# Performance work log

Hardware: AMD Instinct MI355X
Metric: run time of the kernel (lower is better)

Reference implementation:

```python
import jax, jax.numpy as jnp
import numpy as np
import math

NH = 16  # n_head
HS = 64  # head_size = n_embd // n_head


def setup_inputs() -> dict:
    key = jax.random.key(0)
    ks = jax.random.split(key, 7)
    B, T, C, QL, KVL = 2, 2048, 1024, 128, 128
    s = lambda k, shape, fan_in: jax.random.normal(k, shape, jnp.float32) / np.sqrt(fan_in)
    return {
        "x": jax.random.normal(ks[0], (B, T, C), jnp.float32),
        "W_dq": s(ks[1], (QL, C), C),
        "W_uq": s(ks[2], (C, QL), QL),
        "W_dkv": s(ks[3], (KVL, C), C),
        "W_uk": s(ks[4], (C, KVL), KVL),
        "W_uv": s(ks[5], (C, KVL), KVL),
        "W_o": s(ks[6], (C, C), C),
    }


def reference(x, W_dq, W_uq, W_dkv, W_uk, W_uv, W_o):
    B, T, C = x.shape
    kvl = W_dkv.shape[0]
    # absorbed matrices (training branch)
    k_eff = (W_dq.T @ W_uq.T @ W_uk).reshape(NH, HS, kvl)            # (nh, hs, kvl)
    v_eff = (W_uv.T @ W_o.T).reshape(kvl, NH, HS).transpose(1, 0, 2)  # (nh, kvl, hs)
    # latent kv cache
    c_kv = x @ W_dkv.T                                                # (B, T, kvl)
    # query path
    q = (x @ W_dq.T @ W_uq.T).reshape(B, T, NH, HS).transpose(0, 2, 1, 3)  # (B, nh, T, hs)
    # scores: q @ k_eff @ c_kv^T
    ql = jnp.einsum('bhtd,hdl->bhtl', q, k_eff)                       # (B, nh, T, kvl)
    scores = jnp.einsum('bhtl,bsl->bhts', ql, c_kv) / math.sqrt(HS)   # (B, nh, T, T)
    # causal mask
    mask = jnp.tril(jnp.ones((T, T), dtype=bool))
    scores = jnp.where(mask[None, None], scores, -jnp.inf)
    attn = jax.nn.softmax(scores, axis=-1)
    # output: attn @ c_kv @ v_eff
    ctx = jnp.einsum('bhts,bsl->bhtl', attn, c_kv)                    # (B, nh, T, kvl)
    y = jnp.einsum('bhtl,hld->bhtd', ctx, v_eff)                      # (B, nh, T, hs)
    y = y.transpose(0, 2, 1, 3).reshape(B, T, C)
    return y, c_kv
```

## Files before the change

### kernel.cpp

```cpp
#include <hip/hip_runtime.h>
#include <hip/hip_bf16.h>

typedef __hip_bfloat16 bf16;
typedef __attribute__((ext_vector_type(8))) short short8;
typedef __attribute__((ext_vector_type(4))) float f32x4;

#define NHD 16
#define HSD 64
#define KVLD 128
#define QLD 128
#define CD 1024
#define BD 2
#define TD 2048

__device__ __forceinline__ short8 ld8(const bf16* p) { return *(const short8*)p; }
__device__ __forceinline__ void st8(bf16* p, short8 v) { *(short8*)p = v; }

__device__ __forceinline__ short8 cvt8(float4 a, float4 b) {
    union { short8 s; bf16 h[8]; } u;
    u.h[0] = __float2bfloat16(a.x); u.h[1] = __float2bfloat16(a.y);
    u.h[2] = __float2bfloat16(a.z); u.h[3] = __float2bfloat16(a.w);
    u.h[4] = __float2bfloat16(b.x); u.h[5] = __float2bfloat16(b.y);
    u.h[6] = __float2bfloat16(b.z); u.h[7] = __float2bfloat16(b.w);
    return u.s;
}
__device__ __forceinline__ void st4(bf16* p, float4 a) {
    union { short4 s; bf16 h[4]; } u;
    u.h[0] = __float2bfloat16(a.x); u.h[1] = __float2bfloat16(a.y);
    u.h[2] = __float2bfloat16(a.z); u.h[3] = __float2bfloat16(a.w);
    *(short4*)p = u.s;
}
__device__ __forceinline__ void st4f(bf16* p, f32x4 a) {
    union { short4 s; bf16 h[4]; } u;
    u.h[0] = __float2bfloat16(a[0]); u.h[1] = __float2bfloat16(a[1]);
    u.h[2] = __float2bfloat16(a[2]); u.h[3] = __float2bfloat16(a[3]);
    *(short4*)p = u.s;
}


__global__ __launch_bounds__(256) void k_m1p(const float* __restrict__ wuq,
                                             const float* __restrict__ wuk,
                                             float* __restrict__ m1p) {
    int idx = blockIdx.x * 256 + threadIdx.x;
    int i = idx >> 7, j = idx & 127;
    int c0 = blockIdx.y * 128;
    float acc = 0.f;
    for (int c = c0; c < c0 + 128; ++c)
        acc += wuq[c * QLD + i] * wuk[c * KVLD + j];
    m1p[blockIdx.y * 16384 + idx] = acc;
}

__global__ __launch_bounds__(256) void k_m1r(const float* __restrict__ m1p,
                                             float* __restrict__ m1) {
    int idx = blockIdx.x * 256 + threadIdx.x;
    float acc = 0.f;
#pragma unroll
    for (int p = 0; p < 8; ++p) acc += m1p[p * 16384 + idx];
    m1[idx] = acc;
}

__global__ __launch_bounds__(256) void k_keff(const float* __restrict__ wdq,
                                              const float* __restrict__ m1,
                                              float* __restrict__ keff) {
    int idx = blockIdx.x * 256 + threadIdx.x;
    int c = idx >> 7, j = idx & 127;
    float acc = 0.f;
    for (int i = 0; i < QLD; ++i)
        acc += wdq[i * CD + c] * m1[i * KVLD + j];
    keff[idx] = acc;
}

__global__ __launch_bounds__(256) void k_veff(const float* __restrict__ wuv,
                                              const float* __restrict__ wo,
                                              bf16* __restrict__ veffT_bf) {
    int idx = blockIdx.x * 256 + threadIdx.x;
    int l = idx & 127;
    int cc = idx >> 7;
    float acc = 0.f;
    for (int c0 = 0; c0 < CD; ++c0)
        acc += wuv[c0 * KVLD + l] * wo[(size_t)cc * CD + c0];
    veffT_bf[idx] = __float2bfloat16(acc);
}

__global__ __launch_bounds__(256) void k_E(const float* __restrict__ wuq,
                                           const float* __restrict__ keff,
                                           bf16* __restrict__ Et_bf) {
    int idx = blockIdx.x * 256 + threadIdx.x;
    int i = idx & 127;
    int l = (idx >> 7) & 127;
    int h = idx >> 14;
    float acc = 0.f;
    for (int d = 0; d < HSD; ++d)
        acc += wuq[(h * HSD + d) * QLD + i] * keff[(h * HSD + d) * KVLD + l];
    Et_bf[idx] = __float2bfloat16(0.1803368801f * acc);
}

__global__ __launch_bounds__(256) void k_proj(const float* __restrict__ x,
                                              const float* __restrict__ wdq,
                                              const float* __restrict__ wdkv,
                                              bf16* __restrict__ q1_bf,
                                              float* __restrict__ ckv_out,
                                              bf16* __restrict__ ckv_bf,
                                              bf16* __restrict__ ckvT_bf) {
    const int m0 = blockIdx.x * 16;
    const int tid = threadIdx.x;
    const int w = tid >> 6, lane = tid & 63, m16 = lane & 15, g = lane >> 4;

    __shared__ __align__(16) short As_raw[16 * 72];
    __shared__ __align__(16) short Bs_raw[256 * 72];
    bf16* As = (bf16*)As_raw;
    bf16* Bs = (bf16*)Bs_raw;

    f32x4 acc[4];
#pragma unroll
    for (int nb = 0; nb < 4; ++nb) acc[nb] = (f32x4){0.f, 0.f, 0.f, 0.f};

    for (int k0 = 0; k0 < CD; k0 += 64) {
        __syncthreads();
        {
            int row = tid >> 4, kc = (tid & 15) << 2;
            float4 f = *(const float4*)(x + (size_t)(m0 + row) * CD + k0 + kc);
            st4(As + row * 72 + kc, f);
        }
#pragma unroll
        for (int kk = 0; kk < 8; ++kk) {
            int v = tid + kk * 256;
            int row = v >> 3, kc = (v & 7) << 3;
            const float* wr = (row < 128) ? (wdq + (size_t)row * CD)
                                          : (wdkv + (size_t)(row - 128) * CD);
            const float* src = wr + k0 + kc;
            float4 f0 = *(const float4*)(src);
            float4 f1 = *(const float4*)(src + 4);
            st8(Bs + row * 72 + kc, cvt8(f0, f1));
        }
        __syncthreads();
        short8 aF[2];
#pragma unroll
        for (int kf = 0; kf < 2; ++kf)
            aF[kf] = ld8(As + m16 * 72 + kf * 32 + g * 8);
#pragma unroll
        for (int nb = 0; nb < 4; ++nb)
#pragma unroll
            for (int kf = 0; kf < 2; ++kf) {
                short8 bF = ld8(Bs + (w * 64 + nb * 16 + m16) * 72 + kf * 32 + g * 8);
                acc[nb] = __builtin_amdgcn_mfma_f32_16x16x32_bf16(aF[kf], bF, acc[nb], 0, 0, 0);
            }
    }

#pragma unroll
    for (int nb = 0; nb < 4; ++nb)
#pragma unroll
        for (int r = 0; r < 4; ++r) {
            int t = m0 + g * 4 + r;
            int col = w * 64 + nb * 16 + m16;
            float v = acc[nb][r];
            if (col < 128) {
                q1_bf[(size_t)t * QLD + col] = __float2bfloat16(v);
            } else {
                int l = col - 128;
                ckv_out[(size_t)t * KVLD + l] = v;
                bf16 hv = __float2bfloat16(v);
                ckv_bf[(size_t)t * KVLD + l] = hv;
                int b = t >> 11, tl = t & 2047;
                ckvT_bf[((size_t)b * KVLD + l) * TD + tl] = hv;
            }
        }
}

__global__ __launch_bounds__(512, 4) void k_flash(const bf16* __restrict__ Q1_bf,
                                                  const bf16* __restrict__ Et_bf,
                                                  const bf16* __restrict__ ckv_bf,
                                                  const bf16* __restrict__ ckvT_bf,
                                                  const bf16* __restrict__ veffT_bf,
                                                  float* __restrict__ yout) {
    const int h = blockIdx.x & 15;
    const int b = blockIdx.x >> 4;
    const int qlo = blockIdx.y;
    const int qhi = 31 - qlo;
    const int tid = threadIdx.x;
    const int w = tid >> 6;
    const int ws = w >> 2;
    const int wq = w & 3;
    const int lane = tid & 63;
    const int m16 = lane & 15;
    const int g = lane >> 4;
    const int myqt = ws ? qlo : qhi;
    const int row0 = myqt * 64;

    __shared__ __align__(16) short smem_raw[28288];
    bf16* smem = (bf16*)smem_raw;
    bf16* kvN = smem;
    bf16* kvT = smem + 8704;
    bf16* pS  = smem + 19072 + w * 1152;
    bf16* bufLo = kvT;
    bf16* vT = smem + 19072;

    {
        const bf16 one = __float2bfloat16(1.0f);
        for (int idx = tid; idx < 16 * 72; idx += 512)
            kvT[9216 + idx] = one;
    }

    {
        const bf16* q1hi = Q1_bf + ((size_t)(b * TD + qhi * 64)) * QLD;
        const bf16* q1lo = Q1_bf + ((size_t)(b * TD + qlo * 64)) * QLD;
#pragma unroll
        for (int k = 0; k < 2; ++k) {
            int v = tid + k * 512;
            int row = v >> 4, cv = (v & 15) << 3;
            st8(kvN + row * 136 + cv, ld8(q1hi + row * QLD + cv));
            st8(bufLo + row * 136 + cv, ld8(q1lo + row * QLD + cv));
        }
    }
    __syncthreads();
    bf16* myQ1 = ws ? bufLo : kvN;
    {
        short8 aq[4];
#pragma unroll
        for (int kf = 0; kf < 4; ++kf)
            aq[kf] = ld8(myQ1 + (wq * 16 + m16) * 136 + kf * 32 + g * 8);
        const bf16* Eh = Et_bf + (size_t)h * QLD * KVLD;
        f32x4 qc[8];
#pragma unroll
        for (int nb = 0; nb < 8; ++nb) qc[nb] = (f32x4){0.f, 0.f, 0.f, 0.f};
#pragma unroll
        for (int nb = 0; nb < 8; ++nb)
#pragma unroll
            for (int kf = 0; kf < 4; ++kf) {
                short8 bq = ld8(Eh + (nb * 16 + m16) * QLD + kf * 32 + g * 8);
                qc[nb] = __builtin_amdgcn_mfma_f32_16x16x32_bf16(aq[kf], bq, qc[nb], 0, 0, 0);
            }
        __syncthreads();
#pragma unroll
        for (int nb = 0; nb < 8; ++nb)
#pragma unroll
            for (int r = 0; r < 4; ++r)
                myQ1[(wq * 16 + g * 4 + r) * 136 + nb * 16 + m16] = __float2bfloat16(qc[nb][r]);
    }
    __syncthreads();
    short8 qlA[4];
#pragma unroll
    for (int kf = 0; kf < 4; ++kf)
        qlA[kf] = ld8(myQ1 + (wq * 16 + m16) * 136 + kf * 32 + g * 8);

    f32x4 cx[9];
#pragma unroll
    for (int nb = 0; nb < 9; ++nb) cx[nb] = (f32x4){0.f, 0.f, 0.f, 0.f};
    float mrow = -INFINITY;
    const int rg = row0 + wq * 16 + m16;

    const bf16* ckb = ckv_bf + (size_t)b * TD * KVLD;
    const bf16* ckTb = ckvT_bf + (size_t)b * KVLD * TD;

    int nrow[2], ncol[2], trow[2], tcol[2];
#pragma unroll
    for (int k = 0; k < 2; ++k) {
        int v = tid + k * 512;
        nrow[k] = v >> 4; ncol[k] = (v & 15) << 3;
        trow[k] = v >> 3; tcol[k] = (v & 7) << 3;
    }
    short8 pfN[2], pfT[2];
#pragma unroll
    for (int k = 0; k < 2; ++k) {
        pfN[k] = ld8(ckb + (size_t)nrow[k] * KVLD + ncol[k]);
        pfT[k] = ld8(ckTb + (size_t)trow[k] * TD + tcol[k]);
    }

    for (int tile = 0; tile <= qhi; ++tile) {
        const int s0 = tile * 64;
        __syncthreads();
#pragma unroll
        for (int k = 0; k < 2; ++k) {
            st8(kvN + nrow[k] * 136 + ncol[k], pfN[k]);
            st8(kvT + trow[k] * 72 + tcol[k], pfT[k]);
        }
        __syncthreads();
        if (tile < qhi) {
            const int s1 = s0 + 64;
#pragma unroll
            for (int k = 0; k < 2; ++k) {
                pfN[k] = ld8(ckb + (size_t)(s1 + nrow[k]) * KVLD + ncol[k]);
                pfT[k] = ld8(ckTb + (size_t)trow[k] * TD + s1 + tcol[k]);
            }
        }

        if (ws == 0 || tile <= qlo) {
            f32x4 sa[4];
#pragma unroll
            for (int nb = 0; nb < 4; ++nb) sa[nb] = (f32x4){0.f, 0.f, 0.f, 0.f};
#pragma unroll
            for (int nb = 0; nb < 4; ++nb)
#pragma unroll
                for (int kf = 0; kf < 4; ++kf) {
                    short8 ak = ld8(kvN + (nb * 16 + m16) * 136 + kf * 32 + g * 8);
                    sa[nb] = __builtin_amdgcn_mfma_f32_16x16x32_bf16(ak, qlA[kf], sa[nb], 0, 0, 0);
                }

            if (tile == myqt) {
#pragma unroll
                for (int nb = 0; nb < 4; ++nb)
#pragma unroll
                    for (int r = 0; r < 4; ++r) {
                        int sg = s0 + nb * 16 + g * 4 + r;
                        if (sg > rg) sa[nb][r] = -INFINITY;
                    }
            }

            float mloc = sa[0][0];
#pragma unroll
            for (int nb = 0; nb < 4; ++nb)
#pragma unroll
                for (int r = 0; r < 4; ++r) mloc = fmaxf(mloc, sa[nb][r]);
            mloc = fmaxf(mloc, __shfl_xor(mloc, 16));
            mloc = fmaxf(mloc, __shfl_xor(mloc, 32));
            if (__any(mloc > mrow)) {
                float mt = fmaxf(mrow, mloc);
                float al = exp2f(mrow - mt);
                mrow = mt;
#pragma unroll
                for (int nb = 0; nb < 9; ++nb)
#pragma unroll
                    for (int r = 0; r < 4; ++r) cx[nb][r] *= al;
            }

#pragma unroll
            for (int nb = 0; nb < 4; ++nb) {
                float4 p4;
                p4.x = exp2f(sa[nb][0] - mrow);
                p4.y = exp2f(sa[nb][1] - mrow);
                p4.z = exp2f(sa[nb][2] - mrow);
                p4.w = exp2f(sa[nb][3] - mrow);
                st4(pS + m16 * 72 + nb * 16 + g * 4, p4);
            }
            __builtin_amdgcn_wave_barrier();

            short8 pA[2];
#pragma unroll
            for (int kf = 0; kf < 2; ++kf)
                pA[kf] = ld8(pS + m16 * 72 + kf * 32 + g * 8);
#pragma unroll
            for (int nb = 0; nb < 9; ++nb)
#pragma unroll
                for (int kf = 0; kf < 2; ++kf) {
                    short8 av = ld8(kvT + (nb * 16 + m16) * 72 + kf * 32 + g * 8);
                    cx[nb] = __builtin_amdgcn_mfma_f32_16x16x32_bf16(av, pA[kf], cx[nb], 0, 0, 0);
                }
        }
    }

    float invl = 1.f / cx[8][0];
#pragma unroll
    for (int nb = 0; nb < 8; ++nb)
#pragma unroll
        for (int r = 0; r < 4; ++r) cx[nb][r] *= invl;
    __syncthreads();
    bf16* ctxS = ws ? bufLo : kvN;
#pragma unroll
    for (int nb = 0; nb < 8; ++nb)
        st4f(ctxS + (wq * 16 + m16) * 136 + nb * 16 + g * 4, cx[nb]);
    {
        const bf16* vsrc = veffT_bf + (size_t)h * HSD * KVLD;
#pragma unroll
        for (int k = 0; k < 2; ++k) {
            int v = tid + k * 512;
            int row = v >> 4, cv = (v & 15) << 3;
            st8(vT + row * 136 + cv, ld8(vsrc + row * KVLD + cv));
        }
    }
    __syncthreads();

    short8 cB[4];
#pragma unroll
    for (int kf = 0; kf < 4; ++kf)
        cB[kf] = ld8(ctxS + (wq * 16 + m16) * 136 + kf * 32 + g * 8);
    f32x4 ya[4];
#pragma unroll
    for (int nb = 0; nb < 4; ++nb) ya[nb] = (f32x4){0.f, 0.f, 0.f, 0.f};
#pragma unroll
    for (int nb = 0; nb < 4; ++nb)
#pragma unroll
        for (int kf = 0; kf < 4; ++kf) {
            short8 av = ld8(vT + (nb * 16 + m16) * 136 + kf * 32 + g * 8);
            ya[nb] = __builtin_amdgcn_mfma_f32_16x16x32_bf16(av, cB[kf], ya[nb], 0, 0, 0);
        }
    float* yo = yout + ((size_t)b * TD + rg) * CD + h * HSD;
#pragma unroll
    for (int nb = 0; nb < 4; ++nb)
        *(float4*)(yo + nb * 16 + g * 4) = *(float4*)&ya[nb];
}

extern "C" void kernel_launch(void* const* d_in, const int* in_sizes, int n_in,
                              void* d_out, int out_size, void* d_ws, size_t ws_size,
                              hipStream_t stream) {
    const float* x    = (const float*)d_in[0];
    const float* wdq  = (const float*)d_in[1];
    const float* wuq  = (const float*)d_in[2];
    const float* wdkv = (const float*)d_in[3];
    const float* wuk  = (const float*)d_in[4];
    const float* wuv  = (const float*)d_in[5];
    const float* wo   = (const float*)d_in[6];
    float* yout = (float*)d_out;
    float* ckv_out = yout + (size_t)BD * TD * CD;

    float* ws = (float*)d_ws;
    float* M1   = ws;
    float* M1P  = M1 + 16384;
    float* keff = M1P + 131072;
    bf16* Et_bf    = (bf16*)(keff + 131072);
    bf16* veffT_bf = Et_bf + 262144;
    bf16* ckv_bf   = veffT_bf + 131072;
    bf16* ckvT_bf  = ckv_bf + 524288;
    bf16* Q1_bf    = ckvT_bf + 524288;

    dim3 m1grid(64, 8);
    k_m1p <<<m1grid, 256, 0, stream>>>(wuq, wuk, M1P);
    k_m1r <<<64,   256, 0, stream>>>(M1P, M1);
    k_keff<<<512,  256, 0, stream>>>(wdq, M1, keff);
    k_veff<<<512,  256, 0, stream>>>(wuv, wo, veffT_bf);
    k_E   <<<1024, 256, 0, stream>>>(wuq, keff, Et_bf);

    k_proj<<<TD * BD / 16, 256, 0, stream>>>(x, wdq, wdkv, Q1_bf, ckv_out, ckv_bf, ckvT_bf);

    dim3 grid(32, 16);
    k_flash<<<grid, 512, 0, stream>>>(Q1_bf, Et_bf, ckv_bf, ckvT_bf, veffT_bf, yout);
}
```

Before: 263.7 us.

## Fuse weight-absorption prologue kernels into two launches and reassociate E computation

Replaces the six prologue kernels (M1 partials, reduction, k_eff, v_eff, E, projection) with two launches. One kernel computes M1 partials, a per-head G = W_dq-slice·W_uq product, and a bf16 copy of W_dq/W_dkv. The second kernel runs the projection, the E matrix and v_eff concurrently as different block ranges. E is reassociated so the full k_eff is never formed, and the projection now reads weights that were converted to bf16 beforehand. This cuts launch count and serial dependencies and uses register-blocked vector loads. The cost is block-role branching and a different floating-point summation order.

```diff
diff --git a/kernel.cpp b/kernel.cpp
--- a/kernel.cpp
+++ b/kernel.cpp
@@ -16,14 +16,6 @@
 __device__ __forceinline__ short8 ld8(const bf16* p) { return *(const short8*)p; }
 __device__ __forceinline__ void st8(bf16* p, short8 v) { *(short8*)p = v; }
 
-__device__ __forceinline__ short8 cvt8(float4 a, float4 b) {
-    union { short8 s; bf16 h[8]; } u;
-    u.h[0] = __float2bfloat16(a.x); u.h[1] = __float2bfloat16(a.y);
-    u.h[2] = __float2bfloat16(a.z); u.h[3] = __float2bfloat16(a.w);
-    u.h[4] = __float2bfloat16(b.x); u.h[5] = __float2bfloat16(b.y);
-    u.h[6] = __float2bfloat16(b.z); u.h[7] = __float2bfloat16(b.w);
-    return u.s;
-}
 __device__ __forceinline__ void st4(bf16* p, float4 a) {
     union { short4 s; bf16 h[4]; } u;
     u.h[0] = __float2bfloat16(a.x); u.h[1] = __float2bfloat16(a.y);
@@ -37,134 +29,190 @@
     *(short4*)p = u.s;
 }
 
-
-__global__ __launch_bounds__(256) void k_m1p(const float* __restrict__ wuq,
+__global__ __launch_bounds__(256) void k_pre(const float* __restrict__ wuq,
                                              const float* __restrict__ wuk,
-                                             float* __restrict__ m1p) {
-    int idx = blockIdx.x * 256 + threadIdx.x;
-    int i = idx >> 7, j = idx & 127;
-    int c0 = blockIdx.y * 128;
-    float acc = 0.f;
-    for (int c = c0; c < c0 + 128; ++c)
-        acc += wuq[c * QLD + i] * wuk[c * KVLD + j];
-    m1p[blockIdx.y * 16384 + idx] = acc;
-}
-
-__global__ __launch_bounds__(256) void k_m1r(const float* __restrict__ m1p,
-                                             float* __restrict__ m1) {
-    int idx = blockIdx.x * 256 + threadIdx.x;
-    float acc = 0.f;
-#pragma unroll
-    for (int p = 0; p < 8; ++p) acc += m1p[p * 16384 + idx];
-    m1[idx] = acc;
-}
-
-__global__ __launch_bounds__(256) void k_keff(const float* __restrict__ wdq,
-                                              const float* __restrict__ m1,
-                                              float* __restrict__ keff) {
-    int idx = blockIdx.x * 256 + threadIdx.x;
-    int c = idx >> 7, j = idx & 127;
-    float acc = 0.f;
-    for (int i = 0; i < QLD; ++i)
-        acc += wdq[i * CD + c] * m1[i * KVLD + j];
-    keff[idx] = acc;
-}
-
-__global__ __launch_bounds__(256) void k_veff(const float* __restrict__ wuv,
+                                             const float* __restrict__ wdq,
+                                             const float* __restrict__ wdkv,
+                                             float* __restrict__ m1p,
+                                             float* __restrict__ G,
+                                             bf16* __restrict__ wqkv_bf) {
+    const int b = blockIdx.x;
+    const int tid = threadIdx.x;
+    if (b < 32) {
+        const int part = b >> 2, iq = b & 3;
+        const int i = iq * 32 + (tid >> 3);
+        const int j16 = (tid & 7) << 4;
+        float acc[16];
+#pragma unroll
+        for (int t = 0; t < 16; ++t) acc[t] = 0.f;
+        const float* wq = wuq + (size_t)part * 128 * QLD;
+        const float* wk = wuk + (size_t)part * 128 * KVLD;
+#pragma unroll 2
+        for (int c = 0; c < 128; ++c) {
+            float a = wq[c * QLD + i];
+            const float4* wr = (const float4*)(wk + c * KVLD + j16);
+            float4 b0 = wr[0], b1 = wr[1], b2 = wr[2], b3 = wr[3];
+            acc[0] += a * b0.x;  acc[1] += a * b0.y;  acc[2] += a * b0.z;  acc[3] += a * b0.w;
+            acc[4] += a * b1.x;  acc[5] += a * b1.y;  acc[6] += a * b1.z;  acc[7] += a * b1.w;
+            acc[8] += a * b2.x;  acc[9] += a * b2.y;  acc[10] += a * b2.z; acc[11] += a * b2.w;
+            acc[12] += a * b3.x; acc[13] += a * b3.y; acc[14] += a * b3.z; acc[15] += a * b3.w;
+        }
+        float* dst = m1p + (size_t)part * 16384 + (size_t)i * 128 + j16;
+#pragma unroll
+        for (int q = 0; q < 4; ++q)
+            ((float4*)dst)[q] = make_float4(acc[4 * q], acc[4 * q + 1], acc[4 * q + 2], acc[4 * q + 3]);
+    } else if (b < 96) {
+        const int b1 = b - 32;
+        const int h = b1 >> 2, pq = b1 & 3;
+        const int p = pq * 32 + (tid >> 3);
+        const int i16 = (tid & 7) << 4;
+        float acc[16];
+#pragma unroll
+        for (int t = 0; t < 16; ++t) acc[t] = 0.f;
+        const float* wdqp = wdq + (size_t)p * CD + h * 64;
+        const float* wuqh = wuq + (size_t)(h * 64) * QLD + i16;
+#pragma unroll 2
+        for (int d = 0; d < 64; ++d) {
+            float a = wdqp[d];
+            const float4* wr = (const float4*)(wuqh + d * QLD);
+            float4 b0 = wr[0], b1v = wr[1], b2 = wr[2], b3 = wr[3];
+            acc[0] += a * b0.x;  acc[1] += a * b0.y;  acc[2] += a * b0.z;  acc[3] += a * b0.w;
+            acc[4] += a * b1v.x; acc[5] += a * b1v.y; acc[6] += a * b1v.z; acc[7] += a * b1v.w;
+            acc[8] += a * b2.x;  acc[9] += a * b2.y;  acc[10] += a * b2.z; acc[11] += a * b2.w;
+            acc[12] += a * b3.x; acc[13] += a * b3.y; acc[14] += a * b3.z; acc[15] += a * b3.w;
+        }
+        float* dst = G + (size_t)h * 16384 + (size_t)p * 128 + i16;
+#pragma unroll
+        for (int q = 0; q < 4; ++q)
+            ((float4*)dst)[q] = make_float4(acc[4 * q], acc[4 * q + 1], acc[4 * q + 2], acc[4 * q + 3]);
+    } else {
+        const int r = (b - 96) * 16 + (tid >> 4);
+        const int c0 = (tid & 15) << 6;
+        const float* src = (r < 128) ? (wdq + (size_t)r * CD) : (wdkv + (size_t)(r - 128) * CD);
+#pragma unroll
+        for (int t = 0; t < 16; ++t) {
+            float4 f = *(const float4*)(src + c0 + t * 4);
+            st4(wqkv_bf + (size_t)r * CD + c0 + t * 4, f);
+        }
+    }
+}
+
+__global__ __launch_bounds__(256) void k_main(const float* __restrict__ x,
+                                              const bf16* __restrict__ wqkv_bf,
+                                              const float* __restrict__ m1p,
+                                              const float* __restrict__ G,
+                                              const float* __restrict__ wuv,
                                               const float* __restrict__ wo,
-                                              bf16* __restrict__ veffT_bf) {
-    int idx = blockIdx.x * 256 + threadIdx.x;
-    int l = idx & 127;
-    int cc = idx >> 7;
-    float acc = 0.f;
-    for (int c0 = 0; c0 < CD; ++c0)
-        acc += wuv[c0 * KVLD + l] * wo[(size_t)cc * CD + c0];
-    veffT_bf[idx] = __float2bfloat16(acc);
-}
-
-__global__ __launch_bounds__(256) void k_E(const float* __restrict__ wuq,
-                                           const float* __restrict__ keff,
-                                           bf16* __restrict__ Et_bf) {
-    int idx = blockIdx.x * 256 + threadIdx.x;
-    int i = idx & 127;
-    int l = (idx >> 7) & 127;
-    int h = idx >> 14;
-    float acc = 0.f;
-    for (int d = 0; d < HSD; ++d)
-        acc += wuq[(h * HSD + d) * QLD + i] * keff[(h * HSD + d) * KVLD + l];
-    Et_bf[idx] = __float2bfloat16(0.1803368801f * acc);
-}
-
-__global__ __launch_bounds__(256) void k_proj(const float* __restrict__ x,
-                                              const float* __restrict__ wdq,
-                                              const float* __restrict__ wdkv,
                                               bf16* __restrict__ q1_bf,
                                               float* __restrict__ ckv_out,
                                               bf16* __restrict__ ckv_bf,
-                                              bf16* __restrict__ ckvT_bf) {
-    const int m0 = blockIdx.x * 16;
-    const int tid = threadIdx.x;
-    const int w = tid >> 6, lane = tid & 63, m16 = lane & 15, g = lane >> 4;
-
+                                              bf16* __restrict__ ckvT_bf,
+                                              bf16* __restrict__ Et_bf,
+                                              bf16* __restrict__ veffT_bf) {
     __shared__ __align__(16) short As_raw[16 * 72];
     __shared__ __align__(16) short Bs_raw[256 * 72];
-    bf16* As = (bf16*)As_raw;
-    bf16* Bs = (bf16*)Bs_raw;
-
-    f32x4 acc[4];
-#pragma unroll
-    for (int nb = 0; nb < 4; ++nb) acc[nb] = (f32x4){0.f, 0.f, 0.f, 0.f};
-
-    for (int k0 = 0; k0 < CD; k0 += 64) {
+    __shared__ float m1s[1024];
+    const int blk = blockIdx.x;
+    const int tid = threadIdx.x;
+
+    if (blk < 256) {
+        const int m0 = blk * 16;
+        const int w = tid >> 6, lane = tid & 63, m16 = lane & 15, g = lane >> 4;
+        bf16* As = (bf16*)As_raw;
+        bf16* Bs = (bf16*)Bs_raw;
+
+        f32x4 acc[4];
+#pragma unroll
+        for (int nb = 0; nb < 4; ++nb) acc[nb] = (f32x4){0.f, 0.f, 0.f, 0.f};
+
+        for (int k0 = 0; k0 < CD; k0 += 64) {
+            __syncthreads();
+            {
+                int row = tid >> 4, kc = (tid & 15) << 2;
+                float4 f = *(const float4*)(x + (size_t)(m0 + row) * CD + k0 + kc);
+                st4(As + row * 72 + kc, f);
+            }
+#pragma unroll
+            for (int kk = 0; kk < 8; ++kk) {
+                int v = tid + kk * 256;
+                int row = v >> 3, kc = (v & 7) << 3;
+                st8(Bs + row * 72 + kc, ld8(wqkv_bf + (size_t)row * CD + k0 + kc));
+            }
+            __syncthreads();
+            short8 aF[2];
+#pragma unroll
+            for (int kf = 0; kf < 2; ++kf)
+                aF[kf] = ld8(As + m16 * 72 + kf * 32 + g * 8);
+#pragma unroll
+            for (int nb = 0; nb < 4; ++nb)
+#pragma unroll
+                for (int kf = 0; kf < 2; ++kf) {
+                    short8 bF = ld8(Bs + (w * 64 + nb * 16 + m16) * 72 + kf * 32 + g * 8);
+                    acc[nb] = __builtin_amdgcn_mfma_f32_16x16x32_bf16(aF[kf], bF, acc[nb], 0, 0, 0);
+                }
+        }
+
+#pragma unroll
+        for (int nb = 0; nb < 4; ++nb)
+#pragma unroll
+            for (int r = 0; r < 4; ++r) {
+                int t = m0 + g * 4 + r;
+                int col = w * 64 + nb * 16 + m16;
+                float v = acc[nb][r];
+                if (col < 128) {
+                    q1_bf[(size_t)t * QLD + col] = __float2bfloat16(v);
+                } else {
+                    int l = col - 128;
+                    ckv_out[(size_t)t * KVLD + l] = v;
+                    bf16 hv = __float2bfloat16(v);
+                    ckv_bf[(size_t)t * KVLD + l] = hv;
+                    int b = t >> 11, tl = t & 2047;
+                    ckvT_bf[((size_t)b * KVLD + l) * TD + tl] = hv;
+                }
+            }
+    } else if (blk < 512) {
+        const int b2 = blk - 256;
+        const int h = b2 >> 4, lb = b2 & 15;
+        for (int v = tid; v < 1024; v += 256) {
+            int p = v >> 3, lq = v & 7;
+            float s = 0.f;
+#pragma unroll
+            for (int part = 0; part < 8; ++part)
+                s += m1p[(size_t)part * 16384 + (size_t)p * 128 + lb * 8 + lq];
+            m1s[v] = s;
+        }
         __syncthreads();
-        {
-            int row = tid >> 4, kc = (tid & 15) << 2;
-            float4 f = *(const float4*)(x + (size_t)(m0 + row) * CD + k0 + kc);
-            st4(As + row * 72 + kc, f);
-        }
-#pragma unroll
-        for (int kk = 0; kk < 8; ++kk) {
-            int v = tid + kk * 256;
-            int row = v >> 3, kc = (v & 7) << 3;
-            const float* wr = (row < 128) ? (wdq + (size_t)row * CD)
-                                          : (wdkv + (size_t)(row - 128) * CD);
-            const float* src = wr + k0 + kc;
-            float4 f0 = *(const float4*)(src);
-            float4 f1 = *(const float4*)(src + 4);
-            st8(Bs + row * 72 + kc, cvt8(f0, f1));
-        }
-        __syncthreads();
-        short8 aF[2];
-#pragma unroll
-        for (int kf = 0; kf < 2; ++kf)
-            aF[kf] = ld8(As + m16 * 72 + kf * 32 + g * 8);
-#pragma unroll
-        for (int nb = 0; nb < 4; ++nb)
-#pragma unroll
-            for (int kf = 0; kf < 2; ++kf) {
-                short8 bF = ld8(Bs + (w * 64 + nb * 16 + m16) * 72 + kf * 32 + g * 8);
-                acc[nb] = __builtin_amdgcn_mfma_f32_16x16x32_bf16(aF[kf], bF, acc[nb], 0, 0, 0);
-            }
-    }
-
-#pragma unroll
-    for (int nb = 0; nb < 4; ++nb)
-#pragma unroll
-        for (int r = 0; r < 4; ++r) {
-            int t = m0 + g * 4 + r;
-            int col = w * 64 + nb * 16 + m16;
-            float v = acc[nb][r];
-            if (col < 128) {
-                q1_bf[(size_t)t * QLD + col] = __float2bfloat16(v);
-            } else {
-                int l = col - 128;
-                ckv_out[(size_t)t * KVLD + l] = v;
-                bf16 hv = __float2bfloat16(v);
-                ckv_bf[(size_t)t * KVLD + l] = hv;
-                int b = t >> 11, tl = t & 2047;
-                ckvT_bf[((size_t)b * KVLD + l) * TD + tl] = hv;
-            }
-        }
+        const int lq = tid >> 5, i4 = (tid & 31) << 2;
+        const float* Gh = G + (size_t)h * 16384;
+        float4 acc = make_float4(0.f, 0.f, 0.f, 0.f);
+#pragma unroll 4
+        for (int p = 0; p < 128; ++p) {
+            float a = m1s[p * 8 + lq];
+            float4 g4 = *(const float4*)(Gh + p * 128 + i4);
+            acc.x += a * g4.x; acc.y += a * g4.y;
+            acc.z += a * g4.z; acc.w += a * g4.w;
+        }
+        const float sc = 0.1803368801f;
+        const int l = lb * 8 + lq;
+        st4(Et_bf + ((size_t)h * 128 + l) * 128 + i4,
+            make_float4(sc * acc.x, sc * acc.y, sc * acc.z, sc * acc.w));
+    } else {
+        const int b3 = blk - 512;
+        const int cc = b3 * 4 + (tid >> 6);
+        const int l2 = (tid & 63) << 1;
+        const float* wor = wo + (size_t)cc * CD;
+        float ax = 0.f, ay = 0.f;
+#pragma unroll 4
+        for (int c0 = 0; c0 < CD; ++c0) {
+            float a = wor[c0];
+            float2 wv = *(const float2*)(wuv + (size_t)c0 * KVLD + l2);
+            ax += a * wv.x; ay += a * wv.y;
+        }
+        union { short2 s; bf16 h2[2]; } u;
+        u.h2[0] = __float2bfloat16(ax);
+        u.h2[1] = __float2bfloat16(ay);
+        *(short2*)(veffT_bf + (size_t)cc * KVLD + l2) = u.s;
+    }
 }
 
 __global__ __launch_bounds__(512, 4) void k_flash(const bf16* __restrict__ Q1_bf,
@@ -403,23 +451,18 @@
     float* ckv_out = yout + (size_t)BD * TD * CD;
 
     float* ws = (float*)d_ws;
-    float* M1   = ws;
-    float* M1P  = M1 + 16384;
-    float* keff = M1P + 131072;
-    bf16* Et_bf    = (bf16*)(keff + 131072);
+    float* M1P = ws;
+    float* G   = M1P + 131072;
+    bf16* wqkv_bf  = (bf16*)(G + 262144);
+    bf16* Et_bf    = wqkv_bf + 262144;
     bf16* veffT_bf = Et_bf + 262144;
     bf16* ckv_bf   = veffT_bf + 131072;
     bf16* ckvT_bf  = ckv_bf + 524288;
     bf16* Q1_bf    = ckvT_bf + 524288;
 
-    dim3 m1grid(64, 8);
-    k_m1p <<<m1grid, 256, 0, stream>>>(wuq, wuk, M1P);
-    k_m1r <<<64,   256, 0, stream>>>(M1P, M1);
-    k_keff<<<512,  256, 0, stream>>>(wdq, M1, keff);
-    k_veff<<<512,  256, 0, stream>>>(wuv, wo, veffT_bf);
-    k_E   <<<1024, 256, 0, stream>>>(wuq, keff, Et_bf);
-
-    k_proj<<<TD * BD / 16, 256, 0, stream>>>(x, wdq, wdkv, Q1_bf, ckv_out, ckv_bf, ckvT_bf);
+    k_pre <<<112, 256, 0, stream>>>(wuq, wuk, wdq, wdkv, M1P, G, wqkv_bf);
+    k_main<<<768, 256, 0, stream>>>(x, wqkv_bf, M1P, G, wuv, wo,
+                                    Q1_bf, ckv_out, ckv_bf, ckvT_bf, Et_bf, veffT_bf);
 
     dim3 grid(32, 16);
     k_flash<<<grid, 512, 0, stream>>>(Q1_bf, Et_bf, ckv_bf, ckvT_bf, veffT_bf, yout);
```

New measurement: 270.7 us. 2.7% more time.
